# Optimization experiments

Measured on AMD Instinct MI355X. Metric: run time of the kernel, lower is better.

The kernel has to match this reference:

```python
import jax, jax.numpy as jnp
import numpy as np

USER_NUM = 50000
ITEM_NUM = 50000
N_NODES = USER_NUM + ITEM_NUM
EMB = 64
N_LAYERS = 3
ADJ_NNZ = 1600000
S_NNZ = 800000


def spmm(rows, cols, vals, x, n_rows):
    # COO sparse @ dense: out[r] += vals[e] * x[cols[e]]
    gathered = vals[:, None] * x[cols]            # [nnz, d]
    return jax.ops.segment_sum(gathered, rows, num_segments=n_rows)


def setup_inputs() -> dict:
    key = jax.random.key(0)
    ks = jax.random.split(key, 8)
    user_emb = jax.random.normal(ks[0], (USER_NUM, EMB), dtype=jnp.float32) * 0.1
    item_emb = jax.random.normal(ks[1], (ITEM_NUM, EMB), dtype=jnp.float32) * 0.1
    adj_rows = jax.random.randint(ks[2], (ADJ_NNZ,), 0, N_NODES, dtype=jnp.int32)
    adj_cols = jax.random.randint(ks[3], (ADJ_NNZ,), 0, N_NODES, dtype=jnp.int32)
    # values scaled ~ 1/avg_degree so propagation stays well-conditioned (mimics sym-normalized adj)
    adj_vals = jax.random.uniform(ks[4], (ADJ_NNZ,), dtype=jnp.float32) / 16.0
    s_rows = jax.random.randint(ks[5], (S_NNZ,), 0, USER_NUM, dtype=jnp.int32)
    s_cols = jax.random.randint(ks[6], (S_NNZ,), 0, USER_NUM, dtype=jnp.int32)
    s_vals = jax.random.uniform(ks[7], (S_NNZ,), dtype=jnp.float32) / 16.0
    return {"user_emb": user_emb, "item_emb": item_emb,
            "adj_rows": adj_rows, "adj_cols": adj_cols, "adj_vals": adj_vals,
            "s_rows": s_rows, "s_cols": s_cols, "s_vals": s_vals}


def reference(user_emb, item_emb, adj_rows, adj_cols, adj_vals, s_rows, s_cols, s_vals):
    ego = jnp.concatenate([user_emb, item_emb], axis=0)  # [N, d]
    acc = ego
    for _ in range(N_LAYERS):
        u, v = ego[:USER_NUM], ego[USER_NUM:]
        u = u + spmm(s_rows, s_cols, s_vals, u, USER_NUM)
        ego = jnp.concatenate([u, v], axis=0)
        ego = spmm(adj_rows, adj_cols, adj_vals, ego, N_NODES)
        acc = acc + ego
    all_emb = acc / jnp.asarray(N_LAYERS + 1, dtype=acc.dtype)  # mean over layer stack
    return all_emb[:USER_NUM], all_emb[USER_NUM:]
```

## Files before the change

### kernel.cpp

```cpp
#include <hip/hip_runtime.h>


constexpr int USER_NUM = 50000;
constexpr int ITEM_NUM = 50000;
constexpr int N_NODES  = USER_NUM + ITEM_NUM;
constexpr int EMB      = 64;
constexpr int N_LAYERS = 3;
constexpr int TOTAL    = N_NODES * EMB;
constexpr int TOTAL4   = TOTAL / 4;
constexpr int U4       = USER_NUM * EMB / 4;

constexpr int RSHIFT = 10;
constexpr int RB     = 1 << RSHIFT;
constexpr int KA = (N_NODES + RB - 1) / RB;
constexpr int KS = (USER_NUM + RB - 1) / RB;
constexpr int NBIN = 128;
constexpr int BCHUNK = 2048;
constexpr int SLOT   = 17408;

__device__ __forceinline__ int   ntl(const int* p)   { return __builtin_nontemporal_load(p); }
__device__ __forceinline__ float ntlf(const float* p){ return __builtin_nontemporal_load(p); }

__device__ __forceinline__ unsigned f2bf(float f) {
    unsigned b = __float_as_uint(f);
    return (b + 0x7fffu + ((b >> 16) & 1u)) >> 16;
}
__device__ __forceinline__ void bf2x(unsigned u, float& a, float& b) {
    a = __uint_as_float(u << 16);
    b = __uint_as_float(u & 0xffff0000u);
}

__global__ void __launch_bounds__(256) build_and_init(
    const float* __restrict__ user_emb, const float* __restrict__ item_emb,
    unsigned* __restrict__ ego2, int nbin_blocks,
    const int* __restrict__ arows, const int* __restrict__ acols,
    const float* __restrict__ avals, int annz, int nchA, int* __restrict__ tailA,
    int* __restrict__ auxRA, int* __restrict__ auxCA, float* __restrict__ auxVA,
    const int* __restrict__ srows, const int* __restrict__ scols,
    const float* __restrict__ svals, int snnz, int* __restrict__ tailS,
    int* __restrict__ auxRS, int* __restrict__ auxCS, float* __restrict__ auxVS)
{
    __shared__ int hcnt[NBIN], hoff[NBIN], hcur[NBIN], hbase[NBIN];
    __shared__ int sR[BCHUNK], sC[BCHUNK];
    __shared__ float sV[BCHUNK];

    if ((int)blockIdx.x >= nbin_blocks) {
        int i = (blockIdx.x - nbin_blocks) * 256 + threadIdx.x;
        if (i >= TOTAL4) return;
        float4 v = (i < U4) ? reinterpret_cast<const float4*>(user_emb)[i]
                            : reinterpret_cast<const float4*>(item_emb)[i - U4];
        uint2 o;
        o.x = f2bf(v.x) | (f2bf(v.y) << 16);
        o.y = f2bf(v.z) | (f2bf(v.w) << 16);
        reinterpret_cast<uint2*>(ego2)[i] = o;
        return;
    }

    const int* rows; const int* cols; const float* vals; int nnz; int* tail;
    int* auxR; int* auxC; float* auxV; int chunk;
    if ((int)blockIdx.x < nchA) {
        rows = arows; cols = acols; vals = avals; nnz = annz; tail = tailA;
        auxR = auxRA; auxC = auxCA; auxV = auxVA; chunk = blockIdx.x;
    } else {
        rows = srows; cols = scols; vals = svals; nnz = snnz; tail = tailS;
        auxR = auxRS; auxC = auxCS; auxV = auxVS; chunk = blockIdx.x - nchA;
    }
    int begE = chunk * BCHUNK;
    int cnt = nnz - begE; if (cnt > BCHUNK) cnt = BCHUNK;
    int t = threadIdx.x;
    if (t < NBIN) hcnt[t] = 0;
    __syncthreads();
    int r[8], c[8]; float v[8];
    for (int k = 0; k < 8; ++k) {
        int idx = t + k * 256;
        if (idx < cnt) {
            int e = begE + idx;
            r[k] = ntl(rows + e); c[k] = ntl(cols + e); v[k] = ntlf(vals + e);
            atomicAdd(&hcnt[r[k] >> RSHIFT], 1);
        }
    }
    __syncthreads();
    if (t == 0) {
        int run = 0;
        for (int b = 0; b < NBIN; ++b) { hoff[b] = run; hcur[b] = run; run += hcnt[b]; }
    }
    __syncthreads();
    for (int k = 0; k < 8; ++k) {
        int idx = t + k * 256;
        if (idx < cnt) {
            int b = r[k] >> RSHIFT;
            int pos = atomicAdd(&hcur[b], 1);
            sR[pos] = r[k]; sC[pos] = c[k]; sV[pos] = v[k];
        }
    }
    __syncthreads();
    if (t < NBIN && hcnt[t] > 0) hbase[t] = atomicAdd(&tail[t], hcnt[t]);
    __syncthreads();
    for (int idx = t; idx < cnt; idx += 256) {
        int b = sR[idx] >> RSHIFT;
        int g = b * SLOT + hbase[b] + (idx - hoff[b]);
        auxR[g] = sR[idx]; auxC[g] = sC[idx]; auxV[g] = sV[idx];
    }
}

__global__ void __launch_bounds__(1024) bucket_fused(
    const int* __restrict__ auxRA, const int* __restrict__ auxCA,
    const float* __restrict__ auxVA, const int* __restrict__ tailA,
    int* __restrict__ ptrA, int2* __restrict__ packA,
    const int* __restrict__ auxRS, const int* __restrict__ auxCS,
    const float* __restrict__ auxVS, const int* __restrict__ tailS,
    int* __restrict__ ptrS, int2* __restrict__ packS)
{
    __shared__ int cur[RB];
    __shared__ int wsum[16];
    __shared__ int s_pbase;
    const int* auxR; const int* auxC; const float* auxV; const int* tail;
    int* ptr; int2* pack; int b; int n; int K;
    if ((int)blockIdx.x < KA) {
        auxR = auxRA; auxC = auxCA; auxV = auxVA; tail = tailA;
        ptr = ptrA; pack = packA; b = blockIdx.x; n = N_NODES; K = KA;
    } else {
        auxR = auxRS; auxC = auxCS; auxV = auxVS; tail = tailS;
        ptr = ptrS; pack = packS; b = blockIdx.x - KA; n = USER_NUM; K = KS;
    }
    int t = threadIdx.x;
    if (t < 64) {
        int v = (t < b) ? tail[t] : 0;
        if (t + 64 < b) v += tail[t + 64];
        for (int off = 32; off; off >>= 1) v += __shfl_xor(v, off, 64);
        if (t == 0) {
            s_pbase = v;
            if (b == K - 1) ptr[n] = v + tail[b];
        }
    }
    cur[t] = 0;
    __syncthreads();
    int rowbase = b << RSHIFT;
    int nrows = n - rowbase; if (nrows > RB) nrows = RB;
    int cntb = tail[b];
    int segb = b * SLOT, sege = segb + cntb;
    int pbase = s_pbase;
    for (int idx = segb + t; idx < sege; idx += 1024)
        atomicAdd(&cur[ntl(auxR + idx) - rowbase], 1);
    __syncthreads();
    int a0 = cur[t];
    int lane = t & 63, wid = t >> 6;
    int s = a0;
    for (int off = 1; off < 64; off <<= 1) {
        int u = __shfl_up(s, off, 64);
        if (lane >= off) s += u;
    }
    if (lane == 63) wsum[wid] = s;
    __syncthreads();
    if (wid == 0) {
        int w = (lane < 16) ? wsum[lane] : 0;
        for (int off = 1; off < 16; off <<= 1) {
            int u = __shfl_up(w, off, 64);
            if (lane >= off) w += u;
        }
        if (lane < 16) wsum[lane] = w;
    }
    __syncthreads();
    int wbase = (wid > 0) ? wsum[wid - 1] : 0;
    int base = pbase + wbase + s - a0;
    cur[t] = base;
    if (t < nrows) ptr[rowbase + t] = base;
    __syncthreads();
    for (int idx = segb + t; idx < sege; idx += 1024) {
        int rr = ntl(auxR + idx);
        int pos = atomicAdd(&cur[rr - rowbase], 1);
        pack[pos] = make_int2(ntl(auxC + idx), __float_as_int(ntlf(auxV + idx)));
    }
}

__device__ __forceinline__ void gacc(float (&acc)[8], float v, uint4 u) {
    float f0, f1, f2, f3, f4, f5, f6, f7;
    bf2x(u.x, f0, f1); bf2x(u.y, f2, f3); bf2x(u.z, f4, f5); bf2x(u.w, f6, f7);
    acc[0] += v * f0; acc[1] += v * f1; acc[2] += v * f2; acc[3] += v * f3;
    acc[4] += v * f4; acc[5] += v * f5; acc[6] += v * f6; acc[7] += v * f7;
}
__device__ __forceinline__ uint4 pack8(const float (&acc)[8]) {
    uint4 o;
    o.x = f2bf(acc[0]) | (f2bf(acc[1]) << 16);
    o.y = f2bf(acc[2]) | (f2bf(acc[3]) << 16);
    o.z = f2bf(acc[4]) | (f2bf(acc[5]) << 16);
    o.w = f2bf(acc[6]) | (f2bf(acc[7]) << 16);
    return o;
}

__global__ void __launch_bounds__(256) spmm_s(
    const int* __restrict__ ptr, const int2* __restrict__ pack,
    const uint4* __restrict__ ego8, uint4* __restrict__ hu8)
{
    int lane = threadIdx.x & 63;
    int g = (lane >> 3) & 1;
    int li = lane & 7;
    int r = blockIdx.x * 16 + (threadIdx.x >> 6) * 4 + (lane >> 4);
    int beg = 0, end = 0;
    if (r < USER_NUM) { beg = ptr[r]; end = ptr[r + 1]; }
    float acc[8] = {0, 0, 0, 0, 0, 0, 0, 0};
    int j = beg + g;
    for (; j + 2 < end; j += 4) {
        int2 p0 = pack[j];
        int2 p1 = pack[j + 2];
        uint4 x0 = ego8[p0.x * 8 + li];
        uint4 x1 = ego8[p1.x * 8 + li];
        gacc(acc, __int_as_float(p0.y), x0);
        gacc(acc, __int_as_float(p1.y), x1);
    }
    if (j < end) {
        int2 p = pack[j];
        gacc(acc, __int_as_float(p.y), ego8[p.x * 8 + li]);
    }
#pragma unroll
    for (int k = 0; k < 8; ++k) acc[k] += __shfl_xor(acc[k], 8, 64);
    if (g == 0 && r < USER_NUM) {
        uint4 e = ego8[r * 8 + li];
        float f0, f1;
        bf2x(e.x, f0, f1); acc[0] += f0; acc[1] += f1;
        bf2x(e.y, f0, f1); acc[2] += f0; acc[3] += f1;
        bf2x(e.z, f0, f1); acc[4] += f0; acc[5] += f1;
        bf2x(e.w, f0, f1); acc[6] += f0; acc[7] += f1;
        hu8[r * 8 + li] = pack8(acc);
    }
}

template <bool LAST>
__global__ void __launch_bounds__(256) spmm_adj(
    const int* __restrict__ ptr, const int2* __restrict__ pack,
    const uint4* __restrict__ hu8, const uint4* __restrict__ ego8,
    uint4* __restrict__ next8,
    const uint4* __restrict__ e1, const uint4* __restrict__ e2,
    const float* __restrict__ user_emb, const float* __restrict__ item_emb,
    float* __restrict__ accOut)
{
    int lane = threadIdx.x & 63;
    int g = (lane >> 3) & 1;
    int li = lane & 7;
    int r = blockIdx.x * 16 + (threadIdx.x >> 6) * 4 + (lane >> 4);
    int beg = 0, end = 0;
    if (r < N_NODES) { beg = ptr[r]; end = ptr[r + 1]; }
    float acc[8] = {0, 0, 0, 0, 0, 0, 0, 0};
    int j = beg + g;
    for (; j + 2 < end; j += 4) {
        int2 p0 = pack[j];
        int2 p1 = pack[j + 2];
        uint4 x0 = (p0.x < USER_NUM) ? hu8[p0.x * 8 + li] : ego8[p0.x * 8 + li];
        uint4 x1 = (p1.x < USER_NUM) ? hu8[p1.x * 8 + li] : ego8[p1.x * 8 + li];
        gacc(acc, __int_as_float(p0.y), x0);
        gacc(acc, __int_as_float(p1.y), x1);
    }
    if (j < end) {
        int2 p = pack[j];
        uint4 x = (p.x < USER_NUM) ? hu8[p.x * 8 + li] : ego8[p.x * 8 + li];
        gacc(acc, __int_as_float(p.y), x);
    }
#pragma unroll
    for (int k = 0; k < 8; ++k) acc[k] += __shfl_xor(acc[k], 8, 64);
    if (g == 0 && r < N_NODES) {
        if (!LAST) {
            next8[r * 8 + li] = pack8(acc);
        } else {
            const float4* inp; int base;
            if (r < USER_NUM) {
                inp = reinterpret_cast<const float4*>(user_emb);
                base = r * 16 + li * 2;
            } else {
                inp = reinterpret_cast<const float4*>(item_emb);
                base = (r - USER_NUM) * 16 + li * 2;
            }
            float4 v0 = inp[base], v1 = inp[base + 1];
            uint4 a = e1[r * 8 + li];
            uint4 b = e2[r * 8 + li];
            float f0, f1;
            bf2x(a.x, f0, f1); v0.x += f0; v0.y += f1;
            bf2x(a.y, f0, f1); v0.z += f0; v0.w += f1;
            bf2x(a.z, f0, f1); v1.x += f0; v1.y += f1;
            bf2x(a.w, f0, f1); v1.z += f0; v1.w += f1;
            bf2x(b.x, f0, f1); v0.x += f0; v0.y += f1;
            bf2x(b.y, f0, f1); v0.z += f0; v0.w += f1;
            bf2x(b.z, f0, f1); v1.x += f0; v1.y += f1;
            bf2x(b.w, f0, f1); v1.z += f0; v1.w += f1;
            v0.x = (v0.x + acc[0]) * 0.25f; v0.y = (v0.y + acc[1]) * 0.25f;
            v0.z = (v0.z + acc[2]) * 0.25f; v0.w = (v0.w + acc[3]) * 0.25f;
            v1.x = (v1.x + acc[4]) * 0.25f; v1.y = (v1.y + acc[5]) * 0.25f;
            v1.z = (v1.z + acc[6]) * 0.25f; v1.w = (v1.w + acc[7]) * 0.25f;
            float4* op = reinterpret_cast<float4*>(accOut);
            op[r * 16 + li * 2]     = v0;
            op[r * 16 + li * 2 + 1] = v1;
        }
    }
}

extern "C" void kernel_launch(void* const* d_in, const int* in_sizes, int n_in,
                              void* d_out, int out_size, void* d_ws, size_t ws_size,
                              hipStream_t stream) {
    const float* user_emb = (const float*)d_in[0];
    const float* item_emb = (const float*)d_in[1];
    const int*   adj_rows = (const int*)d_in[2];
    const int*   adj_cols = (const int*)d_in[3];
    const float* adj_vals = (const float*)d_in[4];
    const int*   s_rows   = (const int*)d_in[5];
    const int*   s_cols   = (const int*)d_in[6];
    const float* s_vals   = (const float*)d_in[7];
    const int adj_nnz = in_sizes[2];
    const int s_nnz   = in_sizes[5];

    float* acc = (float*)d_out;

    char* p = (char*)d_ws;
    auto alloc = [&](size_t bytes) { void* q = p; p += (bytes + 255) & ~(size_t)255; return q; };
    unsigned* egoA = (unsigned*)alloc((size_t)TOTAL * 2);
    unsigned* egoB = (unsigned*)alloc((size_t)TOTAL * 2);
    unsigned* egoC = (unsigned*)alloc((size_t)TOTAL * 2);
    unsigned* hu   = (unsigned*)alloc((size_t)USER_NUM * EMB * 2);
    int*   ptrA  = (int*)alloc((size_t)(N_NODES + 1) * 4);
    int2*  packA = (int2*)alloc((size_t)adj_nnz * 8);
    int*   ptrS  = (int*)alloc((size_t)(USER_NUM + 1) * 4);
    int2*  packS = (int2*)alloc((size_t)s_nnz * 8);
    int*   auxRA = (int*)alloc((size_t)KA * SLOT * 4);
    int*   auxCA = (int*)alloc((size_t)KA * SLOT * 4);
    float* auxVA = (float*)alloc((size_t)KA * SLOT * 4);
    int*   auxRS = (int*)alloc((size_t)KS * SLOT * 4);
    int*   auxCS = (int*)alloc((size_t)KS * SLOT * 4);
    float* auxVS = (float*)alloc((size_t)KS * SLOT * 4);
    int*   tails = (int*)alloc(2 * NBIN * 4);
    int*   tailA = tails;
    int*   tailS = tails + NBIN;

    const int BLK = 256;
    const int ew_grid = (TOTAL4 + BLK - 1) / BLK;
    const int nchA = (adj_nnz + BCHUNK - 1) / BCHUNK;
    const int nchS = (s_nnz + BCHUNK - 1) / BCHUNK;
    const int nbin_blocks = nchA + nchS;

    hipMemsetAsync(tails, 0, 2 * NBIN * sizeof(int), stream);
    build_and_init<<<nbin_blocks + ew_grid, 256, 0, stream>>>(
        user_emb, item_emb, egoA, nbin_blocks,
        adj_rows, adj_cols, adj_vals, adj_nnz, nchA, tailA, auxRA, auxCA, auxVA,
        s_rows, s_cols, s_vals, s_nnz, tailS, auxRS, auxCS, auxVS);
    bucket_fused<<<KA + KS, 1024, 0, stream>>>(
        auxRA, auxCA, auxVA, tailA, ptrA, packA,
        auxRS, auxCS, auxVS, tailS, ptrS, packS);

    unsigned* bufs[3] = {egoA, egoB, egoC};
    const int s_grid   = (USER_NUM + 15) / 16;
    const int adj_grid = (N_NODES + 15) / 16;

    for (int l = 0; l < N_LAYERS; ++l) {
        unsigned* in  = bufs[l % 3];
        unsigned* out = bufs[(l + 1) % 3];
        spmm_s<<<s_grid, BLK, 0, stream>>>(ptrS, packS, (const uint4*)in, (uint4*)hu);
        if (l < N_LAYERS - 1) {
            spmm_adj<false><<<adj_grid, BLK, 0, stream>>>(
                ptrA, packA, (const uint4*)hu, (const uint4*)in, (uint4*)out,
                nullptr, nullptr, nullptr, nullptr, nullptr);
        } else {
            spmm_adj<true><<<adj_grid, BLK, 0, stream>>>(
                ptrA, packA, (const uint4*)hu, (const uint4*)in, nullptr,
                (const uint4*)egoB, (const uint4*)egoC, user_emb, item_emb, acc);
        }
    }
}
```

Baseline: 334.9 us.

## Split CSR bucket build into global row counting, scan, and wide scatter

Per-row counts are now taken with global atomics during the first binning pass. This replaces the shared-memory count-and-scatter in the bucket kernel, which ran on only one 1024-thread block per bin. A light scan kernel computes row pointers, and a separate scatter kernel uses 16 blocks per bin with global atomic cursors, to raise parallelism in the COO-to-CSR conversion. The cost is an extra launch, a larger memset, and contended global atomics in place of LDS atomics.

```diff
diff --git a/kernel.cpp b/kernel.cpp
--- a/kernel.cpp
+++ b/kernel.cpp
@@ -17,6 +17,7 @@
 constexpr int NBIN = 128;
 constexpr int BCHUNK = 2048;
 constexpr int SLOT   = 17408;
+constexpr int FSUB   = 16;
 
 __device__ __forceinline__ int   ntl(const int* p)   { return __builtin_nontemporal_load(p); }
 __device__ __forceinline__ float ntlf(const float* p){ return __builtin_nontemporal_load(p); }
@@ -35,9 +36,11 @@
     unsigned* __restrict__ ego2, int nbin_blocks,
     const int* __restrict__ arows, const int* __restrict__ acols,
     const float* __restrict__ avals, int annz, int nchA, int* __restrict__ tailA,
+    int* __restrict__ rowcntA,
     int* __restrict__ auxRA, int* __restrict__ auxCA, float* __restrict__ auxVA,
     const int* __restrict__ srows, const int* __restrict__ scols,
     const float* __restrict__ svals, int snnz, int* __restrict__ tailS,
+    int* __restrict__ rowcntS,
     int* __restrict__ auxRS, int* __restrict__ auxCS, float* __restrict__ auxVS)
 {
     __shared__ int hcnt[NBIN], hoff[NBIN], hcur[NBIN], hbase[NBIN];
@@ -57,13 +60,13 @@
     }
 
     const int* rows; const int* cols; const float* vals; int nnz; int* tail;
-    int* auxR; int* auxC; float* auxV; int chunk;
+    int* rowcnt; int* auxR; int* auxC; float* auxV; int chunk;
     if ((int)blockIdx.x < nchA) {
         rows = arows; cols = acols; vals = avals; nnz = annz; tail = tailA;
-        auxR = auxRA; auxC = auxCA; auxV = auxVA; chunk = blockIdx.x;
+        rowcnt = rowcntA; auxR = auxRA; auxC = auxCA; auxV = auxVA; chunk = blockIdx.x;
     } else {
         rows = srows; cols = scols; vals = svals; nnz = snnz; tail = tailS;
-        auxR = auxRS; auxC = auxCS; auxV = auxVS; chunk = blockIdx.x - nchA;
+        rowcnt = rowcntS; auxR = auxRS; auxC = auxCS; auxV = auxVS; chunk = blockIdx.x - nchA;
     }
     int begE = chunk * BCHUNK;
     int cnt = nnz - begE; if (cnt > BCHUNK) cnt = BCHUNK;
@@ -77,6 +80,7 @@
             int e = begE + idx;
             r[k] = ntl(rows + e); c[k] = ntl(cols + e); v[k] = ntlf(vals + e);
             atomicAdd(&hcnt[r[k] >> RSHIFT], 1);
+            atomicAdd(&rowcnt[r[k]], 1);
         }
     }
     __syncthreads();
@@ -103,25 +107,21 @@
     }
 }
 
-__global__ void __launch_bounds__(1024) bucket_fused(
-    const int* __restrict__ auxRA, const int* __restrict__ auxCA,
-    const float* __restrict__ auxVA, const int* __restrict__ tailA,
-    int* __restrict__ ptrA, int2* __restrict__ packA,
-    const int* __restrict__ auxRS, const int* __restrict__ auxCS,
-    const float* __restrict__ auxVS, const int* __restrict__ tailS,
-    int* __restrict__ ptrS, int2* __restrict__ packS)
-{
-    __shared__ int cur[RB];
+__global__ void __launch_bounds__(1024) scan_rows(
+    const int* __restrict__ tailA, const int* __restrict__ rowcntA,
+    int* __restrict__ ptrA, int* __restrict__ gcurA,
+    const int* __restrict__ tailS, const int* __restrict__ rowcntS,
+    int* __restrict__ ptrS, int* __restrict__ gcurS)
+{
     __shared__ int wsum[16];
     __shared__ int s_pbase;
-    const int* auxR; const int* auxC; const float* auxV; const int* tail;
-    int* ptr; int2* pack; int b; int n; int K;
+    const int* tail; const int* rowcnt; int* ptr; int* gcur; int b; int n; int K;
     if ((int)blockIdx.x < KA) {
-        auxR = auxRA; auxC = auxCA; auxV = auxVA; tail = tailA;
-        ptr = ptrA; pack = packA; b = blockIdx.x; n = N_NODES; K = KA;
+        tail = tailA; rowcnt = rowcntA; ptr = ptrA; gcur = gcurA;
+        b = blockIdx.x; n = N_NODES; K = KA;
     } else {
-        auxR = auxRS; auxC = auxCS; auxV = auxVS; tail = tailS;
-        ptr = ptrS; pack = packS; b = blockIdx.x - KA; n = USER_NUM; K = KS;
+        tail = tailS; rowcnt = rowcntS; ptr = ptrS; gcur = gcurS;
+        b = blockIdx.x - KA; n = USER_NUM; K = KS;
     }
     int t = threadIdx.x;
     if (t < 64) {
@@ -133,17 +133,9 @@
             if (b == K - 1) ptr[n] = v + tail[b];
         }
     }
-    cur[t] = 0;
-    __syncthreads();
     int rowbase = b << RSHIFT;
-    int nrows = n - rowbase; if (nrows > RB) nrows = RB;
-    int cntb = tail[b];
-    int segb = b * SLOT, sege = segb + cntb;
-    int pbase = s_pbase;
-    for (int idx = segb + t; idx < sege; idx += 1024)
-        atomicAdd(&cur[ntl(auxR + idx) - rowbase], 1);
-    __syncthreads();
-    int a0 = cur[t];
+    int row = rowbase + t;
+    int a0 = (row < n) ? rowcnt[row] : 0;
     int lane = t & 63, wid = t >> 6;
     int s = a0;
     for (int off = 1; off < 64; off <<= 1) {
@@ -162,13 +154,35 @@
     }
     __syncthreads();
     int wbase = (wid > 0) ? wsum[wid - 1] : 0;
-    int base = pbase + wbase + s - a0;
-    cur[t] = base;
-    if (t < nrows) ptr[rowbase + t] = base;
-    __syncthreads();
-    for (int idx = segb + t; idx < sege; idx += 1024) {
-        int rr = ntl(auxR + idx);
-        int pos = atomicAdd(&cur[rr - rowbase], 1);
+    int base = s_pbase + wbase + s - a0;
+    if (row < n) { ptr[row] = base; gcur[row] = base; }
+}
+
+__global__ void __launch_bounds__(256) scatter(
+    const int* __restrict__ auxRA, const int* __restrict__ auxCA,
+    const float* __restrict__ auxVA, const int* __restrict__ tailA,
+    int* __restrict__ gcurA, int2* __restrict__ packA,
+    const int* __restrict__ auxRS, const int* __restrict__ auxCS,
+    const float* __restrict__ auxVS, const int* __restrict__ tailS,
+    int* __restrict__ gcurS, int2* __restrict__ packS)
+{
+    int bf = blockIdx.x;
+    int b = bf / FSUB, f = bf % FSUB;
+    const int* auxR; const int* auxC; const float* auxV; const int* tail;
+    int* gcur; int2* pack;
+    if (b < KA) {
+        auxR = auxRA; auxC = auxCA; auxV = auxVA; tail = tailA;
+        gcur = gcurA; pack = packA;
+    } else {
+        b -= KA;
+        auxR = auxRS; auxC = auxCS; auxV = auxVS; tail = tailS;
+        gcur = gcurS; pack = packS;
+    }
+    int segb = b * SLOT;
+    int sege = segb + tail[b];
+    for (int idx = segb + f * 256 + (int)threadIdx.x; idx < sege; idx += 256 * FSUB) {
+        int r = ntl(auxR + idx);
+        int pos = atomicAdd(&gcur[r], 1);
         pack[pos] = make_int2(ntl(auxC + idx), __float_as_int(ntlf(auxV + idx)));
     }
 }
@@ -324,9 +338,14 @@
     int*   auxRS = (int*)alloc((size_t)KS * SLOT * 4);
     int*   auxCS = (int*)alloc((size_t)KS * SLOT * 4);
     float* auxVS = (float*)alloc((size_t)KS * SLOT * 4);
-    int*   tails = (int*)alloc(2 * NBIN * 4);
-    int*   tailA = tails;
-    int*   tailS = tails + NBIN;
+    int*   gcurA = (int*)alloc((size_t)N_NODES * 4);
+    int*   gcurS = (int*)alloc((size_t)USER_NUM * 4);
+    constexpr int ZN = 2 * NBIN + N_NODES + USER_NUM;
+    int*   zer    = (int*)alloc((size_t)ZN * 4);
+    int*   tailA  = zer;
+    int*   tailS  = zer + NBIN;
+    int*   rowcntA = zer + 2 * NBIN;
+    int*   rowcntS = rowcntA + N_NODES;
 
     const int BLK = 256;
     const int ew_grid = (TOTAL4 + BLK - 1) / BLK;
@@ -334,14 +353,18 @@
     const int nchS = (s_nnz + BCHUNK - 1) / BCHUNK;
     const int nbin_blocks = nchA + nchS;
 
-    hipMemsetAsync(tails, 0, 2 * NBIN * sizeof(int), stream);
+    hipMemsetAsync(zer, 0, (size_t)ZN * 4, stream);
     build_and_init<<<nbin_blocks + ew_grid, 256, 0, stream>>>(
         user_emb, item_emb, egoA, nbin_blocks,
-        adj_rows, adj_cols, adj_vals, adj_nnz, nchA, tailA, auxRA, auxCA, auxVA,
-        s_rows, s_cols, s_vals, s_nnz, tailS, auxRS, auxCS, auxVS);
-    bucket_fused<<<KA + KS, 1024, 0, stream>>>(
-        auxRA, auxCA, auxVA, tailA, ptrA, packA,
-        auxRS, auxCS, auxVS, tailS, ptrS, packS);
+        adj_rows, adj_cols, adj_vals, adj_nnz, nchA, tailA, rowcntA,
+        auxRA, auxCA, auxVA,
+        s_rows, s_cols, s_vals, s_nnz, tailS, rowcntS,
+        auxRS, auxCS, auxVS);
+    scan_rows<<<KA + KS, 1024, 0, stream>>>(
+        tailA, rowcntA, ptrA, gcurA, tailS, rowcntS, ptrS, gcurS);
+    scatter<<<(KA + KS) * FSUB, 256, 0, stream>>>(
+        auxRA, auxCA, auxVA, tailA, gcurA, packA,
+        auxRS, auxCS, auxVS, tailS, gcurS, packS);
 
     unsigned* bufs[3] = {egoA, egoB, egoC};
     const int s_grid   = (USER_NUM + 15) / 16;
```

After: 476.0 us. 1.42x slower.
